# Optimization experiments

Hardware: AMD Instinct MI355X
Metric: run time of the kernel (lower is better)

The kernel has to match this reference:

```python
import jax, jax.numpy as jnp
import numpy as np

H = 1024
E = 1024
B = 4096
DEPTH = 1


def setup_inputs() -> dict:
    key = jax.random.key(0)
    ks = jax.random.split(key, 12)
    s = 1.0 / np.sqrt(E + 2 * H)
    inp = {
        "X": jax.random.normal(ks[0], (B, E), jnp.float32),
        "index": 0,
        "length": 64,
        "prev_a": jax.random.normal(ks[1], (B, DEPTH + 1, H), jnp.float32),
        "prev_b": jax.random.normal(ks[2], (B, DEPTH + 1, H), jnp.float32),
        "prev_depth": jax.random.randint(ks[3], (B, 1), 0, 2, jnp.int32),
        # torch Linear weights: y = x @ W.T, W shape (out, in)
        "w_a00": jax.random.uniform(ks[4], (H, E + 2 * H), jnp.float32, -s, s),
        "w_a10": jax.random.uniform(ks[5], (H, E + H), jnp.float32, -s, s),
        "w_b00": jax.random.uniform(ks[6], (H, E + 2 * H), jnp.float32, -s, s),
        "w_b11": jax.random.uniform(ks[7], (H, E + H), jnp.float32, -s, s),
        "w_b10": jax.random.uniform(ks[8], (H, E + H), jnp.float32, -s, s),
        "w_b01": jax.random.uniform(ks[9], (H, E + 2 * H), jnp.float32, -s, s),
        "w_att": jax.random.uniform(ks[10], (4, 8 * H), jnp.float32, -s, s),
    }
    return inp


def _gate(pd, cond_val, branch, carry):
    # eq(pd,cond)*branch + gt(pd,cond)*carry + lt(pd,cond)*0
    eq = (pd == cond_val).astype(branch.dtype)
    gt = (pd > cond_val).astype(branch.dtype)
    return eq * branch + gt * carry


def reference(X, index, length, prev_a, prev_b, prev_depth,
              w_a00, w_a10, w_b00, w_b11, w_b10, w_b01, w_att):
    b, h = X.shape[0], prev_b.shape[-1]
    pd = prev_depth.astype(X.dtype)  # (B,1)
    a0, a1 = prev_a[:, 0, :], prev_a[:, 1, :]
    b0, b1 = prev_b[:, 0, :], prev_b[:, 1, :]

    # d = 1 (only depth level)
    nofork_nojoin_a = jnp.concatenate([X, b0, a1], 1) @ w_a00.T
    fork_nojoin_a = jnp.concatenate([X, b0], 1) @ w_a10.T
    na00 = _gate(pd, 1.0, nofork_nojoin_a, a1)
    na11 = _gate(pd, 1.0, a1, a1)                 # fork_join_a = prev_a[:,1]
    na10 = _gate(pd, 0.0, fork_nojoin_a, a1)      # eq(pd+1, 1) <=> pd == 0
    na01 = _gate(pd, 2.0, a0, a1)                 # eq(pd-1, 1) <=> pd == 2

    fork_join_b = jnp.concatenate([X, b1], 1) @ w_b11.T
    nofork_nojoin_b = jnp.concatenate([X, a1, na00], 1) @ w_b00.T
    fork_nojoin_b = jnp.concatenate([X, na10], 1) @ w_b10.T
    nofork_join_b = jnp.concatenate([X, b0, a1], 1) @ w_b01.T
    nb00 = _gate(pd, 1.0, nofork_nojoin_b, b1)
    nb11 = _gate(pd, 1.0, fork_join_b, b1)
    nb10 = _gate(pd, 0.0, fork_nojoin_b, b1)
    nb01 = _gate(pd, 2.0, nofork_join_b, b1)

    zeros2h = jnp.zeros((b, 2 * h), X.dtype)  # d=0 slot of each branch
    f00 = jnp.concatenate([zeros2h, na00, nb00], 1)  # (B, stride=4h)
    f01 = jnp.concatenate([zeros2h, na01, nb01], 1)
    f10 = jnp.concatenate([zeros2h, na10, nb10], 1)
    f11 = jnp.concatenate([zeros2h, na11, nb11], 1)
    state = jnp.stack([f00, f01, f10, f11], 1)  # (B, 4, 4h)

    # attention over next_state_flat[:, depth_size:] == [f10, f11]
    att_in = jnp.concatenate([f10, f11], 1)  # (B, 8h)
    pd0 = pd[:, 0]
    e0 = (pd0 == 0.0).astype(X.dtype)
    e1 = (pd0 == 1.0).astype(X.dtype)
    eD = (pd0 == float(DEPTH)).astype(X.dtype)
    mask = jnp.stack([1 - e0, (1 - e0) * (1 - e1), 1 - eD, 1 - e0], 1)  # (B,4)
    att_vars = mask * jax.nn.softmax(jax.nn.sigmoid(att_in @ w_att.T), axis=1)

    # straight-through argmax: forward one-hot, backward identity
    hard = jax.nn.one_hot(jnp.argmax(att_vars, axis=1), 4, dtype=X.dtype)
    sel = jax.lax.stop_gradient(hard - att_vars) + att_vars

    # bmm with striped identity == select the chosen stripe
    hidden = jnp.einsum('bk,bkd->bd', sel, state).reshape(b, DEPTH + 1, 2 * h)
    next_a = hidden[:, :, :h]
    next_b = hidden[:, :, h:]

    pdi = prev_depth[:, 0]
    hi = hard.astype(prev_depth.dtype)
    next_depth = (hi[:, 0] * pdi + hi[:, 1] * (pdi - 1)
                  + hi[:, 2] * (pdi + 1) + hi[:, 3] * pdi)[:, None]
    f = (sel[:, 2] + sel[:, 3])[:, None]
    j = (sel[:, 1] + sel[:, 3])[:, None]
    return (next_a, next_b, next_depth, f, j)
```

## Files before the change

kernel.cpp:

```cpp
#include <hip/hip_runtime.h>
#include <hip/hip_bf16.h>
#include <stdint.h>
#include <math.h>

typedef unsigned short u16;
typedef __attribute__((ext_vector_type(8))) short frag8;
typedef __attribute__((ext_vector_type(4))) float f32x4;

#define Hdim 1024
#define Brows 4096

#define OUT_B_OFF  8388608
#define OUT_D_OFF 16777216
#define OUT_F_OFF 16781312
#define OUT_J_OFF 16785408

#define CNT_OFF   32768
#define LISTS_OFF 32832
#define BF16_OFF  98304

#define XB      0u
#define B0B     4194304u
#define A1B     8388608u
#define B1B     12582912u
#define NA00B   16777216u
#define NA10B   20971520u
#define WA00B   25165824u
#define WA10B   28311552u
#define WB00B   30408704u
#define WB11B   33554432u
#define WB10B   35651584u
#define WS_BF_ELTS 37748736u
#define WS_NEED ((unsigned long long)BF16_OFF + (unsigned long long)WS_BF_ELTS * 2ull)

#define NO_BCOPY 0xFFFFFFFFu

__device__ __forceinline__ u16 f2bf(float f) {
    union { float f; unsigned int i; } v; v.f = f;
    unsigned int r = v.i + 0x7fffu + ((v.i >> 16) & 1u);
    return (u16)(r >> 16);
}
__device__ __forceinline__ unsigned int pk2(float a, float b) {
    __hip_bfloat162 h = __float22bfloat162_rn(make_float2(a, b));
    union { __hip_bfloat162 h; unsigned int u; } v; v.h = h; return v.u;
}
__device__ __forceinline__ void gl_lds16(const u16* g, u16* l) {
    __builtin_amdgcn_global_load_lds(
        (const __attribute__((address_space(1))) unsigned int*)g,
        (__attribute__((address_space(3))) unsigned int*)l, 16, 0, 0);
}


struct GDesc {
    unsigned int a0, a1s, a2;
    unsigned int w;
    unsigned int bcopy;
    int K;
    const int* rows;
    const int* pcnt;
    float* outp;
};
struct GPack { GDesc d[3]; };

__global__ __launch_bounds__(256)
void gemm_gather(u16* __restrict__ ws16, GPack gp)
{
    __shared__ alignas(16) u16 lsA[2][64 * 64];
    __shared__ alignas(16) u16 lsB[2][64 * 64];

    const GDesc g = gp.d[blockIdx.z];
    const int navail = *g.pcnt;
    const int m0 = blockIdx.x * 64;
    if (m0 >= navail) return;

    const int tid  = threadIdx.x;
    const int lane = tid & 63;
    const int wv   = tid >> 6;
    const int n0   = blockIdx.y * 64;

    int ridx[2];
#pragma unroll
    for (int i = 0; i < 2; ++i) {
        const int mi = m0 + (tid >> 3) + i * 32;
        ridx[i] = (mi < navail) ? g.rows[mi] : 0;
    }

    f32x4 acc[4];
#pragma unroll
    for (int i = 0; i < 4; ++i) acc[i] = (f32x4){0.f, 0.f, 0.f, 0.f};

    const u16* segp[3] = { ws16 + g.a0, ws16 + g.a1s, ws16 + g.a2 };
    const u16* W = ws16 + g.w;
    const int K = g.K;

    const int swz = ((tid & 7) ^ ((tid >> 3) & 7)) * 8;
    const int brow0 = tid >> 3;

    auto STAGE = [&](int buf, int kt) {
        const int seg = kt >> 4;
        const int kl  = (kt & 15) * 64;
        const u16* abase = segp[seg] + kl;
        const u16* wb = W + (size_t)n0 * K + kt * 64;
#pragma unroll
        for (int i = 0; i < 2; ++i)
            gl_lds16(abase + (size_t)ridx[i] * 1024 + swz, &lsA[buf][(i * 256 + tid) * 8]);
#pragma unroll
        for (int i = 0; i < 2; ++i)
            gl_lds16(wb + (size_t)(i * 32 + brow0) * K + swz, &lsB[buf][(i * 256 + tid) * 8]);
    };
    auto COMPUTE = [&](int buf) {
#pragma unroll
        for (int ks = 0; ks < 2; ++ks) {
            const int kb = (ks * 32 + (lane >> 4) * 8) * 2;
            frag8 af[4], bfr;
#pragma unroll
            for (int i = 0; i < 4; ++i) {
                const int ro = i * 16 + (lane & 15);
                af[i] = *(const frag8*)((const char*)lsA[buf] +
                            ((ro * 128 + kb) ^ ((ro & 7) << 4)));
            }
            {
                const int ro = wv * 16 + (lane & 15);
                bfr = *(const frag8*)((const char*)lsB[buf] +
                            ((ro * 128 + kb) ^ ((ro & 7) << 4)));
            }
#pragma unroll
            for (int i = 0; i < 4; ++i)
                acc[i] = __builtin_amdgcn_mfma_f32_16x16x32_bf16(af[i], bfr, acc[i], 0, 0, 0);
        }
    };

    const int nkt = K / 64;
    STAGE(0, 0);
    for (int kt = 0; kt < nkt; ++kt) {
        const int cur = kt & 1;
        if (kt + 1 < nkt) {
            STAGE(cur ^ 1, kt + 1);
            asm volatile("s_waitcnt vmcnt(4)" ::: "memory");
        } else {
            asm volatile("s_waitcnt vmcnt(0)" ::: "memory");
        }
        __builtin_amdgcn_sched_barrier(0);
        __builtin_amdgcn_s_barrier();
        __builtin_amdgcn_sched_barrier(0);
        COMPUTE(cur);
        __builtin_amdgcn_sched_barrier(0);
        __builtin_amdgcn_s_barrier();
    }

    u16* bc = (g.bcopy != NO_BCOPY) ? (ws16 + g.bcopy) : nullptr;
    const int quad = lane >> 4;
    const int lcol = lane & 15;
    const int gcol = n0 + wv * 16 + lcol;
#pragma unroll
    for (int i = 0; i < 4; ++i) {
#pragma unroll
        for (int r = 0; r < 4; ++r) {
            const int mi = m0 + i * 16 + quad * 4 + r;
            if (mi >= navail) continue;
            const int grow = g.rows[mi];
            const float v = acc[i][r];
            if (bc) bc[(size_t)grow * 1024 + gcol] = f2bf(v);
            g.outp[(size_t)grow * 2048 + gcol] = v;
        }
    }
}

__global__ __launch_bounds__(256)
void prep_conv(const float* __restrict__ prev_b,
               const float* __restrict__ wa00, const float* __restrict__ wa10,
               const float* __restrict__ wb00, const float* __restrict__ wb11,
               const float* __restrict__ wb10,
               const float* __restrict__ w_att,
               float* __restrict__ u,
               u16* __restrict__ ws16)
{
    const int bid = blockIdx.x;
    if (bid < 512) {
        const int k  = (bid & 7) * 256 + threadIdx.x;
        const int c0 = (bid >> 3) * 16;
        float s0 = 0.f, s3 = 0.f;
        for (int c = c0; c < c0 + 16; ++c) {
            const float w = wb11[(size_t)c * 2048 + k];
            s0 += w * w_att[7168 + c];
            s3 += w * w_att[3 * 8192 + 7168 + c];
        }
        atomicAdd(&u[k], s0);
        atomicAdd(&u[2048 + k], s3);
        return;
    }
    long long gid = (long long)(bid - 512) * 256 + threadIdx.x;
    const float* src;
    unsigned int dst;
    long long idx;
    if (gid < 786432) {
        idx = gid;               src = wa00 + idx * 4; dst = WA00B;
    } else if (gid < 1310720) {
        idx = gid - 786432;      src = wa10 + idx * 4; dst = WA10B;
    } else if (gid < 2097152) {
        idx = gid - 1310720;     src = wb00 + idx * 4; dst = WB00B;
    } else if (gid < 2621440) {
        idx = gid - 2097152;     src = wb11 + idx * 4; dst = WB11B;
    } else if (gid < 3145728) {
        idx = gid - 2621440;     src = wb10 + idx * 4; dst = WB10B;
    } else {
        idx = gid - 3145728;
        src = prev_b + (idx >> 8) * 2048 + (idx & 255) * 4;          dst = B0B;
    }
    float4 v = *(const float4*)src;
    uint2 h = { pk2(v.x, v.y), pk2(v.z, v.w) };
    *(uint2*)&ws16[(size_t)dst + idx * 4] = h;
}

#define BMf 128
#define BNf 64
#define LDK 72

struct RegTile { float4 a[8]; float4 b[4]; };

__device__ __forceinline__ void load_tile(RegTile& s,
        const float* const* segp, const int* segs,
        const float* __restrict__ W, int K, int kn,
        int m0, int n0, int lr, int lc)
{
    const int seg = kn >> 4;
    const int kl  = (kn & 15) * 64;
    const float* ab = segp[seg];
    const int astr  = segs[seg];
#pragma unroll
    for (int i = 0; i < 8; ++i)
        s.a[i] = *(const float4*)(ab + (size_t)(m0 + i * 16 + lr) * astr + kl + lc);
#pragma unroll
    for (int i = 0; i < 4; ++i)
        s.b[i] = *(const float4*)(W + (size_t)(n0 + i * 16 + lr) * K + kn * 64 + lc);
}
__device__ __forceinline__ void stage_tile(const RegTile& s, u16* LA, u16* LB,
                                           int lr, int lc)
{
#pragma unroll
    for (int i = 0; i < 8; ++i) {
        uint2 h = { pk2(s.a[i].x, s.a[i].y), pk2(s.a[i].z, s.a[i].w) };
        *(uint2*)&LA[(i * 16 + lr) * LDK + lc] = h;
    }
#pragma unroll
    for (int i = 0; i < 4; ++i) {
        uint2 h = { pk2(s.b[i].x, s.b[i].y), pk2(s.b[i].z, s.b[i].w) };
        *(uint2*)&LB[(i * 16 + lr) * LDK + lc] = h;
    }
}
__device__ __forceinline__ void do_mfma_f(const u16* LA, const u16* LB,
                                          int wm, int wn, int lane, f32x4 acc[4][2])
{
#pragma unroll
    for (int ks = 0; ks < 2; ++ks) {
        const int kc = ks * 32 + (lane >> 4) * 8;
        frag8 af[4], bf[2];
#pragma unroll
        for (int i = 0; i < 4; ++i)
            af[i] = *(const frag8*)&LA[(wm * 64 + i * 16 + (lane & 15)) * LDK + kc];
#pragma unroll
        for (int j = 0; j < 2; ++j)
            bf[j] = *(const frag8*)&LB[(wn * 32 + j * 16 + (lane & 15)) * LDK + kc];
#pragma unroll
        for (int i = 0; i < 4; ++i)
#pragma unroll
            for (int j = 0; j < 2; ++j)
                acc[i][j] = __builtin_amdgcn_mfma_f32_16x16x32_bf16(af[i], bf[j], acc[i][j], 0, 0, 0);
    }
}

__global__ __launch_bounds__(256)
void gemm_k(const float* __restrict__ a0, int as0,
            const float* __restrict__ a1p, int as1,
            const float* __restrict__ a2p, int as2,
            const float* __restrict__ W, int K,
            const int* __restrict__ gate, int ksel,
            float* __restrict__ outp, int ostr)
{
    __shared__ alignas(16) u16 lsA[2][BMf * LDK];
    __shared__ alignas(16) u16 lsB[2][BNf * LDK];

    const int tid  = threadIdx.x;
    const int lane = tid & 63;
    const int wv   = tid >> 6;
    const int wm   = wv >> 1, wn = wv & 1;
    const int m0   = blockIdx.x * BMf;
    const int n0   = blockIdx.y * BNf;
    const int lr = tid >> 4;
    const int lc = (tid & 15) * 4;

    f32x4 acc[4][2];
#pragma unroll
    for (int i = 0; i < 4; ++i)
#pragma unroll
        for (int j = 0; j < 2; ++j) acc[i][j] = (f32x4){0.f, 0.f, 0.f, 0.f};

    const float* segp[3] = { a0, a1p, a2p };
    const int    segs[3] = { as0, as1, as2 };

    const int nkt = K / 64;
    RegTile S0, S1;
    load_tile(S0, segp, segs, W, K, 0, m0, n0, lr, lc);
    load_tile(S1, segp, segs, W, K, 1, m0, n0, lr, lc);
    stage_tile(S0, lsA[0], lsB[0], lr, lc);
    __syncthreads();

    for (int kt = 0; kt < nkt; kt += 2) {
        if (kt + 2 < nkt) load_tile(S0, segp, segs, W, K, kt + 2, m0, n0, lr, lc);
        do_mfma_f(lsA[0], lsB[0], wm, wn, lane, acc);
        stage_tile(S1, lsA[1], lsB[1], lr, lc);
        __syncthreads();
        if (kt + 3 < nkt) load_tile(S1, segp, segs, W, K, kt + 3, m0, n0, lr, lc);
        do_mfma_f(lsA[1], lsB[1], wm, wn, lane, acc);
        if (kt + 2 < nkt) {
            stage_tile(S0, lsA[0], lsB[0], lr, lc);
            __syncthreads();
        }
    }

    const int quad = lane >> 4;
    const int lcol = lane & 15;
#pragma unroll
    for (int i = 0; i < 4; ++i) {
#pragma unroll
        for (int r = 0; r < 4; ++r) {
            const int grow = m0 + wm * 64 + i * 16 + quad * 4 + r;
            if (gate[grow] == ksel) {
#pragma unroll
                for (int j = 0; j < 2; ++j) {
                    const int gcol = n0 + wn * 32 + j * 16 + lcol;
                    outp[(size_t)grow * ostr + gcol] = acc[i][j][r];
                }
            }
        }
    }
}

__global__ __launch_bounds__(256)
void prep_u(const float* __restrict__ w_b11, const float* __restrict__ w_att,
            float* __restrict__ u)
{
    const int k  = (blockIdx.x & 7) * 256 + threadIdx.x;
    const int c0 = (blockIdx.x >> 3) * 16;
    float s0 = 0.f, s3 = 0.f;
    for (int c = c0; c < c0 + 16; ++c) {
        const float w = w_b11[(size_t)c * 2048 + k];
        s0 += w * w_att[7168 + c];
        s3 += w * w_att[3 * 8192 + 7168 + c];
    }
    atomicAdd(&u[k], s0);
    atomicAdd(&u[2048 + k], s3);
}

__global__ __launch_bounds__(256)
void decide(const float* __restrict__ X,
            const float* __restrict__ prev_a, const float* __restrict__ prev_b,
            const int* __restrict__ pdin,
            const float* __restrict__ w_att,
            const float* __restrict__ u,
            int* __restrict__ kbuf,
            int* __restrict__ lists,
            int* __restrict__ cnt,
            u16* __restrict__ wsx,
            float* __restrict__ out)
{
    const int lane = threadIdx.x & 63;
    const int wv   = threadIdx.x >> 6;
    const int b    = blockIdx.x * 4 + wv;
    const int pd   = pdin[b];

    const float* a1 = prev_a + (size_t)b * 2048 + 1024;
    const float* b1 = prev_b + (size_t)b * 2048 + 1024;
    const float* xr = X + (size_t)b * 1024;

    int k;
    float fv;
    if (pd == 0) {
        k = 2; fv = 1.f;
    } else {
        float d0 = 0.f, d3 = 0.f;
        const float* w0 = w_att;
        const float* w3 = w_att + 3 * 8192;
        const float* u0 = u;
        const float* u3 = u + 2048;
#pragma unroll
        for (int uu = 0; uu < 2; ++uu) {
            const int c = lane * 16 + uu * 8;
#pragma unroll
            for (int q = 0; q < 2; ++q) {
                const int cc = c + q * 4;
                float4 av = *(const float4*)&a1[cc];
                float4 bv = *(const float4*)&b1[cc];
                float4 xv = *(const float4*)&xr[cc];
                float4 wa0 = *(const float4*)&w0[2048 + cc];
                float4 wb0 = *(const float4*)&w0[3072 + cc];
                float4 wc0 = *(const float4*)&w0[6144 + cc];
                float4 wa3 = *(const float4*)&w3[2048 + cc];
                float4 wb3 = *(const float4*)&w3[3072 + cc];
                float4 wc3 = *(const float4*)&w3[6144 + cc];
                float4 ux0 = *(const float4*)&u0[cc];
                float4 ux3 = *(const float4*)&u3[cc];
                float4 ub0 = *(const float4*)&u0[1024 + cc];
                float4 ub3 = *(const float4*)&u3[1024 + cc];
                d0 += av.x*(wa0.x+wc0.x) + av.y*(wa0.y+wc0.y) + av.z*(wa0.z+wc0.z) + av.w*(wa0.w+wc0.w);
                d3 += av.x*(wa3.x+wc3.x) + av.y*(wa3.y+wc3.y) + av.z*(wa3.z+wc3.z) + av.w*(wa3.w+wc3.w);
                d0 += bv.x*wb0.x + bv.y*wb0.y + bv.z*wb0.z + bv.w*wb0.w;
                d3 += bv.x*wb3.x + bv.y*wb3.y + bv.z*wb3.z + bv.w*wb3.w;
                d0 += xv.x*ux0.x + xv.y*ux0.y + xv.z*ux0.z + xv.w*ux0.w;
                d3 += xv.x*ux3.x + xv.y*ux3.y + xv.z*ux3.z + xv.w*ux3.w;
                d0 += bv.x*ub0.x + bv.y*ub0.y + bv.z*ub0.z + bv.w*ub0.w;
                d3 += bv.x*ub3.x + bv.y*ub3.y + bv.z*ub3.z + bv.w*ub3.w;
            }
        }
#pragma unroll
        for (int off = 32; off; off >>= 1) {
            d0 += __shfl_xor(d0, off, 64);
            d3 += __shfl_xor(d3, off, 64);
        }
        k = (d3 > d0) ? 3 : 0;
        fv = (k == 3) ? 1.f : 0.f;
    }
    const float jv = (pd == 0) ? 0.f : fv;
    const int nd = (k == 2) ? pd + 1 : pd;

    float* outA = out;
    float* outB = out + OUT_B_OFF;

    const float4 z4 = make_float4(0.f, 0.f, 0.f, 0.f);
#pragma unroll
    for (int uu = 0; uu < 4; ++uu) {
        const int c = uu * 256 + lane * 4;
        *(float4*)&outA[(size_t)b * 2048 + c] = z4;
        *(float4*)&outB[(size_t)b * 2048 + c] = z4;
    }
    if (k == 3) {
#pragma unroll
        for (int uu = 0; uu < 4; ++uu) {
            const int c = uu * 256 + lane * 4;
            *(float4*)&outA[(size_t)b * 2048 + 1024 + c] = *(const float4*)&a1[c];
        }
    }
    if (wsx) {
#pragma unroll
        for (int uu = 0; uu < 4; ++uu) {
            const int c = uu * 256 + lane * 4;
            float4 xv = *(const float4*)&xr[c];
            float4 av = *(const float4*)&a1[c];
            float4 bv = *(const float4*)&b1[c];
            uint2 hx = { pk2(xv.x, xv.y), pk2(xv.z, xv.w) };
            uint2 ha = { pk2(av.x, av.y), pk2(av.z, av.w) };
            uint2 hb = { pk2(bv.x, bv.y), pk2(bv.z, bv.w) };
            *(uint2*)&wsx[XB  + (size_t)b * 1024 + c] = hx;
            *(uint2*)&wsx[A1B + (size_t)b * 1024 + c] = ha;
            *(uint2*)&wsx[B1B + (size_t)b * 1024 + c] = hb;
        }
    }
    if (lane == 0) {
        kbuf[b] = k;
        if (lists) {
            const int j = (k == 0) ? 0 : (k == 2) ? 1 : 2;
            const int pos = atomicAdd(&cnt[j], 1);
            lists[j * 4096 + pos] = b;
        }
        out[OUT_D_OFF + b] = (float)nd;
        out[OUT_F_OFF + b] = fv;
        out[OUT_J_OFF + b] = jv;
    }
}

extern "C" void kernel_launch(void* const* d_in, const int* in_sizes, int n_in,
                              void* d_out, int out_size, void* d_ws, size_t ws_size,
                              hipStream_t stream)
{
    const float* X      = (const float*)d_in[0];
    const float* prev_a = (const float*)d_in[3];
    const float* prev_b = (const float*)d_in[4];
    const int*   pd     = (const int*)d_in[5];
    const float* w_a00  = (const float*)d_in[6];
    const float* w_a10  = (const float*)d_in[7];
    const float* w_b00  = (const float*)d_in[8];
    const float* w_b11  = (const float*)d_in[9];
    const float* w_b10  = (const float*)d_in[10];
    const float* w_att  = (const float*)d_in[12];

    float* u     = (float*)d_ws;
    int*   kbuf  = (int*)((char*)d_ws + 16384);
    int*   cnt   = (int*)((char*)d_ws + CNT_OFF);
    int*   lists = (int*)((char*)d_ws + LISTS_OFF);
    u16*   ws16  = (u16*)((char*)d_ws + BF16_OFF);

    const float* a1 = prev_a + 1024;
    const float* b0 = prev_b;
    const float* b1 = prev_b + 1024;

    float* out   = (float*)d_out;
    float* outA1 = out + 1024;
    float* outB1 = out + OUT_B_OFF + 1024;

    dim3 blk(256);
    const bool fast = (ws_size >= WS_NEED);

    if (fast) {
        hipMemsetAsync(d_ws, 0, CNT_OFF + 64, stream);
        prep_conv<<<dim3(512 + 16384), blk, 0, stream>>>(prev_b,
            w_a00, w_a10, w_b00, w_b11, w_b10, w_att, u, ws16);
        decide<<<dim3(Brows / 4), blk, 0, stream>>>(X, prev_a, prev_b, pd, w_att, u,
                                                    kbuf, lists, cnt, ws16, out);

        int* l0 = lists;
        int* l2 = lists + 4096;
        int* l3 = lists + 8192;

        GPack p1;
        p1.d[0] = { XB, B0B, A1B, WA00B, NA00B,    3072, l0, &cnt[0], outA1 };
        p1.d[1] = { XB, B0B, 0u,  WA10B, NA10B,    2048, l2, &cnt[1], outA1 };
        p1.d[2] = { XB, B1B, 0u,  WB11B, NO_BCOPY, 2048, l3, &cnt[2], outB1 };
        gemm_gather<<<dim3(Brows / 64, Hdim / 64, 3), blk, 0, stream>>>(ws16, p1);

        GPack p2;
        p2.d[0] = { XB, A1B,   NA00B, WB00B, NO_BCOPY, 3072, l0, &cnt[0], outB1 };
        p2.d[1] = { XB, NA10B, 0u,    WB10B, NO_BCOPY, 2048, l2, &cnt[1], outB1 };
        p2.d[2] = p2.d[0];
        gemm_gather<<<dim3(Brows / 64, Hdim / 64, 2), blk, 0, stream>>>(ws16, p2);
    } else {
        hipMemsetAsync(u, 0, 16384, stream);
        prep_u<<<dim3(512), blk, 0, stream>>>(w_b11, w_att, u);
        decide<<<dim3(Brows / 4), blk, 0, stream>>>(X, prev_a, prev_b, pd, w_att, u,
                                                    kbuf, nullptr, cnt, nullptr, out);
        dim3 grid(Brows / BMf, Hdim / BNf);
        gemm_k<<<grid, blk, 0, stream>>>(X, 1024, b0, 2048, a1, 2048,
                                         w_a00, 3072, kbuf, 0, outA1, 2048);
        gemm_k<<<grid, blk, 0, stream>>>(X, 1024, b0, 2048, nullptr, 0,
                                         w_a10, 2048, kbuf, 2, outA1, 2048);
        gemm_k<<<grid, blk, 0, stream>>>(X, 1024, b1, 2048, nullptr, 0,
                                         w_b11, 2048, pd, 1, outB1, 2048);
        gemm_k<<<grid, blk, 0, stream>>>(X, 1024, a1, 2048, outA1, 2048,
                                         w_b00, 3072, kbuf, 0, outB1, 2048);
        gemm_k<<<grid, blk, 0, stream>>>(X, 1024, outA1, 2048, nullptr, 0,
                                         w_b10, 2048, kbuf, 2, outB1, 2048);
    }
}
```

Baseline: 350.5 us.

## Split dependent GEMMs so independent K-segments run in the first launch

```diff
diff --git a/kernel.cpp b/kernel.cpp
--- a/kernel.cpp
+++ b/kernel.cpp
@@ -56,17 +56,19 @@
     unsigned int w;
     unsigned int bcopy;
     int K;
+    int Kst;
     const int* rows;
     const int* pcnt;
     float* outp;
+    const float* accp;
 };
-struct GPack { GDesc d[3]; };
+struct GPack { GDesc d[5]; };
 
 __global__ __launch_bounds__(256)
 void gemm_gather(u16* __restrict__ ws16, GPack gp)
 {
-    __shared__ alignas(16) u16 lsA[2][64 * 64];
-    __shared__ alignas(16) u16 lsB[2][64 * 64];
+    __shared__ alignas(16) u16 lsA[64 * 64];
+    __shared__ alignas(16) u16 lsB[64 * 64];
 
     const GDesc g = gp.d[blockIdx.z];
     const int navail = *g.pcnt;
@@ -78,6 +80,10 @@
     const int wv   = tid >> 6;
     const int n0   = blockIdx.y * 64;
 
+    const int quad = lane >> 4;
+    const int lcol = lane & 15;
+    const int gcol = n0 + wv * 16 + lcol;
+
     int ridx[2];
 #pragma unroll
     for (int i = 0; i < 2; ++i) {
@@ -88,27 +94,38 @@
     f32x4 acc[4];
 #pragma unroll
     for (int i = 0; i < 4; ++i) acc[i] = (f32x4){0.f, 0.f, 0.f, 0.f};
+    if (g.accp) {
+#pragma unroll
+        for (int i = 0; i < 4; ++i)
+#pragma unroll
+            for (int r = 0; r < 4; ++r) {
+                const int mi = m0 + i * 16 + quad * 4 + r;
+                if (mi < navail)
+                    acc[i][r] = g.accp[(size_t)g.rows[mi] * 2048 + gcol];
+            }
+    }
 
     const u16* segp[3] = { ws16 + g.a0, ws16 + g.a1s, ws16 + g.a2 };
     const u16* W = ws16 + g.w;
     const int K = g.K;
+    const int Kst = g.Kst;
 
     const int swz = ((tid & 7) ^ ((tid >> 3) & 7)) * 8;
     const int brow0 = tid >> 3;
 
-    auto STAGE = [&](int buf, int kt) {
+    const int nkt = K / 64;
+    for (int kt = 0; kt < nkt; ++kt) {
         const int seg = kt >> 4;
         const int kl  = (kt & 15) * 64;
         const u16* abase = segp[seg] + kl;
-        const u16* wb = W + (size_t)n0 * K + kt * 64;
+        const u16* wb = W + (size_t)n0 * Kst + kt * 64;
 #pragma unroll
         for (int i = 0; i < 2; ++i)
-            gl_lds16(abase + (size_t)ridx[i] * 1024 + swz, &lsA[buf][(i * 256 + tid) * 8]);
+            gl_lds16(abase + (size_t)ridx[i] * 1024 + swz, &lsA[(i * 256 + tid) * 8]);
 #pragma unroll
         for (int i = 0; i < 2; ++i)
-            gl_lds16(wb + (size_t)(i * 32 + brow0) * K + swz, &lsB[buf][(i * 256 + tid) * 8]);
-    };
-    auto COMPUTE = [&](int buf) {
+            gl_lds16(wb + (size_t)(i * 32 + brow0) * Kst + swz, &lsB[(i * 256 + tid) * 8]);
+        __syncthreads();
 #pragma unroll
         for (int ks = 0; ks < 2; ++ks) {
             const int kb = (ks * 32 + (lane >> 4) * 8) * 2;
@@ -116,42 +133,22 @@
 #pragma unroll
             for (int i = 0; i < 4; ++i) {
                 const int ro = i * 16 + (lane & 15);
-                af[i] = *(const frag8*)((const char*)lsA[buf] +
+                af[i] = *(const frag8*)((const char*)lsA +
                             ((ro * 128 + kb) ^ ((ro & 7) << 4)));
             }
             {
                 const int ro = wv * 16 + (lane & 15);
-                bfr = *(const frag8*)((const char*)lsB[buf] +
+                bfr = *(const frag8*)((const char*)lsB +
                             ((ro * 128 + kb) ^ ((ro & 7) << 4)));
             }
 #pragma unroll
             for (int i = 0; i < 4; ++i)
                 acc[i] = __builtin_amdgcn_mfma_f32_16x16x32_bf16(af[i], bfr, acc[i], 0, 0, 0);
         }
-    };
-
-    const int nkt = K / 64;
-    STAGE(0, 0);
-    for (int kt = 0; kt < nkt; ++kt) {
-        const int cur = kt & 1;
-        if (kt + 1 < nkt) {
-            STAGE(cur ^ 1, kt + 1);
-            asm volatile("s_waitcnt vmcnt(4)" ::: "memory");
-        } else {
-            asm volatile("s_waitcnt vmcnt(0)" ::: "memory");
-        }
-        __builtin_amdgcn_sched_barrier(0);
-        __builtin_amdgcn_s_barrier();
-        __builtin_amdgcn_sched_barrier(0);
-        COMPUTE(cur);
-        __builtin_amdgcn_sched_barrier(0);
-        __builtin_amdgcn_s_barrier();
+        __syncthreads();
     }
 
     u16* bc = (g.bcopy != NO_BCOPY) ? (ws16 + g.bcopy) : nullptr;
-    const int quad = lane >> 4;
-    const int lcol = lane & 15;
-    const int gcol = n0 + wv * 16 + lcol;
 #pragma unroll
     for (int i = 0; i < 4; ++i) {
 #pragma unroll
@@ -512,15 +509,19 @@
         int* l3 = lists + 8192;
 
         GPack p1;
-        p1.d[0] = { XB, B0B, A1B, WA00B, NA00B,    3072, l0, &cnt[0], outA1 };
-        p1.d[1] = { XB, B0B, 0u,  WA10B, NA10B,    2048, l2, &cnt[1], outA1 };
-        p1.d[2] = { XB, B1B, 0u,  WB11B, NO_BCOPY, 2048, l3, &cnt[2], outB1 };
-        gemm_gather<<<dim3(Brows / 64, Hdim / 64, 3), blk, 0, stream>>>(ws16, p1);
+        p1.d[0] = { XB, B0B, A1B, WA00B, NA00B,    3072, 3072, l0, &cnt[0], outA1, nullptr };
+        p1.d[1] = { XB, B0B, 0u,  WA10B, NA10B,    2048, 2048, l2, &cnt[1], outA1, nullptr };
+        p1.d[2] = { XB, A1B, 0u,  WB00B, NO_BCOPY, 2048, 3072, l0, &cnt[0], outB1, nullptr };
+        p1.d[3] = { XB, B1B, 0u,  WB11B, NO_BCOPY, 2048, 2048, l3, &cnt[2], outB1, nullptr };
+        p1.d[4] = { XB, 0u,  0u,  WB10B, NO_BCOPY, 1024, 2048, l2, &cnt[1], outB1, nullptr };
+        gemm_gather<<<dim3(Brows / 64, Hdim / 64, 5), blk, 0, stream>>>(ws16, p1);
 
         GPack p2;
-        p2.d[0] = { XB, A1B,   NA00B, WB00B, NO_BCOPY, 3072, l0, &cnt[0], outB1 };
-        p2.d[1] = { XB, NA10B, 0u,    WB10B, NO_BCOPY, 2048, l2, &cnt[1], outB1 };
+        p2.d[0] = { NA00B, 0u, 0u, WB00B + 2048u, NO_BCOPY, 1024, 3072, l0, &cnt[0], outB1, outB1 };
+        p2.d[1] = { NA10B, 0u, 0u, WB10B + 1024u, NO_BCOPY, 1024, 2048, l2, &cnt[1], outB1, outB1 };
         p2.d[2] = p2.d[0];
+        p2.d[3] = p2.d[0];
+        p2.d[4] = p2.d[0];
         gemm_gather<<<dim3(Brows / 64, Hdim / 64, 2), blk, 0, stream>>>(ws16, p2);
     } else {
         hipMemsetAsync(u, 0, 16384, stream);
```

Measured after the change: 341.1 us. 1.03x faster.
